# Performance work log

Measured on AMD Instinct MI355X. Metric: run time of the kernel, lower is better.

The kernel has to match this reference:

```python
import jax, jax.numpy as jnp
import numpy as np

N_GRAPHS = 512
N_PER_G = 84
N = N_GRAPHS * N_PER_G            # 43008 nodes
E = N_GRAPHS * N_PER_G * N_PER_G  # 3612672 edges (fully connected incl. self-loops)


def setup_inputs() -> dict:
    key = jax.random.key(0)
    ks = jax.random.split(key, 10)
    x = jax.random.normal(ks[0], (N, 84), dtype=jnp.float32)
    # fully-connected edge_index per graph: [2, E], row0=src j, row1=dst i
    off = (np.arange(N_GRAPHS) * N_PER_G)[:, None, None]
    src = (off + np.arange(N_PER_G)[:, None]) + np.zeros((1, 1, N_PER_G), np.int64)
    dst = (off + np.arange(N_PER_G)[None, None, :]) + np.zeros((1, N_PER_G, 1), np.int64)
    edge_index = jnp.asarray(np.stack([src.reshape(-1), dst.reshape(-1)]), dtype=jnp.int64)
    batch = jnp.asarray(np.repeat(np.arange(N_GRAPHS), N_PER_G), dtype=jnp.int64)
    s = 0.1
    W1 = jax.random.normal(ks[1], (84, 64), dtype=jnp.float32) * s
    a_src1 = jax.random.normal(ks[2], (32, 2), dtype=jnp.float32) * s
    a_dst1 = jax.random.normal(ks[3], (32, 2), dtype=jnp.float32) * s
    b1 = jnp.zeros((64,), jnp.float32)
    W2 = jax.random.normal(ks[4], (64, 64), dtype=jnp.float32) * s
    a_src2 = jax.random.normal(ks[5], (1, 64), dtype=jnp.float32) * s
    a_dst2 = jax.random.normal(ks[6], (1, 64), dtype=jnp.float32) * s
    b2 = jnp.zeros((64,), jnp.float32)
    Wfc = jax.random.normal(ks[7], (64, 1), dtype=jnp.float32) * s
    bfc = jnp.zeros((1,), jnp.float32)
    return {"x": x, "edge_index": edge_index, "batch": batch,
            "W1": W1, "a_src1": a_src1, "a_dst1": a_dst1, "b1": b1,
            "W2": W2, "a_src2": a_src2, "a_dst2": a_dst2, "b2": b2,
            "Wfc": Wfc, "bfc": bfc}


def gat_conv(x, W, a_src, a_dst, bias, src, dst, n_heads, ch):
    # x: [N, F] -> h: [N, H, C]
    h = (x @ W).reshape(-1, n_heads, ch)
    alpha_src = jnp.sum(h * a_src, axis=-1)  # [N, H]
    alpha_dst = jnp.sum(h * a_dst, axis=-1)  # [N, H]
    e = jax.nn.leaky_relu(alpha_src[src] + alpha_dst[dst], 0.2)  # [E, H]
    # segment softmax over edges grouped by destination node
    m = jax.ops.segment_max(e, dst, num_segments=N)
    e = jnp.exp(e - m[dst])
    z = jax.ops.segment_sum(e, dst, num_segments=N)
    alpha = e / (z[dst] + 1e-16)                              # [E, H]
    msg = h[src] * alpha[:, :, None]                          # [E, H, C]
    out = jax.ops.segment_sum(msg, dst, num_segments=N)       # [N, H, C]
    return out.reshape(-1, n_heads * ch) + bias


def reference(x, edge_index, batch, W1, a_src1, a_dst1, b1, W2, a_src2, a_dst2, b2, Wfc, bfc):
    src, dst = edge_index[0], edge_index[1]
    h = gat_conv(x, W1, a_src1, a_dst1, b1, src, dst, 32, 2)   # [N, 64]
    h = jax.nn.elu(h)
    h = gat_conv(h, W2, a_src2, a_dst2, b2, src, dst, 1, 64)   # [N, 64]
    # global mean pool per graph
    sums = jax.ops.segment_sum(h, batch, num_segments=N_GRAPHS)
    cnts = jax.ops.segment_sum(jnp.ones((N, 1), h.dtype), batch, num_segments=N_GRAPHS)
    pooled = sums / cnts                                       # [B, 64]
    out = pooled @ Wfc + bfc                                   # [B, 1]
    z = jnp.zeros((1,), jnp.float32)
    return (out, z, z, z, z, z, z)
```

## Files before the change

kernel.cpp:

```cpp
#include <hip/hip_runtime.h>

#define NG 512
#define P  84
#define F0 84
#define F1 64
#define L2E 1.4426950408889634f

typedef float f32x2 __attribute__((ext_vector_type(2)));

#if __has_builtin(__builtin_amdgcn_exp2f)
#define EXP2F(v) __builtin_amdgcn_exp2f(v)
#else
#define EXP2F(v) exp2f(v)
#endif
#if __has_builtin(__builtin_amdgcn_rcpf)
#define RCPF(v) __builtin_amdgcn_rcpf(v)
#else
#define RCPF(v) (1.0f / (v))
#endif

__device__ __forceinline__ float rlane(float v, int l) {
  return __int_as_float(__builtin_amdgcn_readlane(__float_as_int(v), l));
}


__launch_bounds__(512, 2)
__global__ void gat_fused(const float* __restrict__ x,
                          const float* __restrict__ W1,
                          const float* __restrict__ a_src1,
                          const float* __restrict__ a_dst1,
                          const float* __restrict__ b1,
                          const float* __restrict__ W2,
                          const float* __restrict__ a_src2,
                          const float* __restrict__ a_dst2,
                          const float* __restrict__ b2,
                          const float* __restrict__ Wfc,
                          const float* __restrict__ bfc,
                          float* __restrict__ out)
{
  __shared__ float  h1s[P * F1];
  __shared__ float  o1s[P * F1];
  __shared__ float  a2s[2 * F1];
  __shared__ float2 as2p[P];
  __shared__ float2 ad2p[P];
  __shared__ float  reds[8 * P];
  __shared__ float  redt[P];

  const int tid = threadIdx.x;
  const int ln  = tid & 63;
  const int wid = tid >> 6;
  const int g   = blockIdx.x;
  const int nrows = (wid < 4) ? 11 : 10;
  const int i0    = (wid < 4) ? wid * 11 : 44 + (wid - 4) * 10;

  if (g == 0 && tid < 6) out[NG + tid] = 0.f;

  const float* xg = x + (size_t)g * P * F0;

  float xr0[11], xr1[11];
  #pragma unroll
  for (int ii = 0; ii < 11; ++ii) {
    int ie = (ii < nrows) ? (i0 + ii) : i0;
    const float* xrow = xg + ie * F0;
    xr0[ii] = xrow[ln];
    xr1[ii] = (ln < F0 - 64) ? xrow[64 + ln] : 0.f;
  }
  if (tid < F1) a2s[tid] = a_src2[tid] * L2E;
  else if (tid < 2 * F1) a2s[tid] = a_dst2[tid - F1] * L2E;

  {
    float acc[11];
    #pragma unroll
    for (int ii = 0; ii < 11; ++ii) acc[ii] = 0.f;
    {
      float wk[42];
      #pragma unroll
      for (int k = 0; k < 42; ++k) wk[k] = W1[k * F1 + ln];
      #pragma unroll
      for (int k = 0; k < 42; ++k) {
        #pragma unroll
        for (int ii = 0; ii < 11; ++ii)
          acc[ii] = fmaf(rlane(xr0[ii], k), wk[k], acc[ii]);
      }
    }
    {
      float wk[42];
      #pragma unroll
      for (int k = 0; k < 42; ++k) wk[k] = W1[(42 + k) * F1 + ln];
      #pragma unroll
      for (int k = 0; k < 22; ++k) {
        #pragma unroll
        for (int ii = 0; ii < 11; ++ii)
          acc[ii] = fmaf(rlane(xr0[ii], 42 + k), wk[k], acc[ii]);
      }
      #pragma unroll
      for (int k = 0; k < 20; ++k) {
        #pragma unroll
        for (int ii = 0; ii < 11; ++ii)
          acc[ii] = fmaf(rlane(xr1[ii], k), wk[22 + k], acc[ii]);
      }
    }
    #pragma unroll
    for (int ii = 0; ii < 11; ++ii)
      if (ii < nrows) h1s[(i0 + ii) * F1 + ln] = acc[ii];
  }
  __syncthreads();

  {
    const int h  = tid & 31;
    const int ig = tid >> 5;
    const float asa = a_src1[2 * h] * L2E, asb = a_src1[2 * h + 1] * L2E;
    const float ada = a_dst1[2 * h] * L2E, adb = a_dst1[2 * h + 1] * L2E;
    f32x2 pi2[3], qi2[3], sm2[3], m02[3], m12[3];
    #pragma unroll
    for (int u = 0; u < 3; ++u) {
      int iA = ig + 16 * (2 * u);     if (iA >= P) iA = P - 1;
      int iB = ig + 16 * (2 * u + 1); if (iB >= P) iB = P - 1;
      float2 cA = *(const float2*)&h1s[iA * F1 + 2 * h];
      float2 cB = *(const float2*)&h1s[iB * F1 + 2 * h];
      float adiA = fmaf(cA.x, ada, cA.y * adb);
      float adiB = fmaf(cB.x, ada, cB.y * adb);
      pi2[u] = (f32x2){EXP2F(adiA), EXP2F(adiB)};
      qi2[u] = (f32x2){EXP2F(0.2f * adiA), EXP2F(0.2f * adiB)};
      sm2[u] = (f32x2){0.f, 0.f};
      m02[u] = (f32x2){0.f, 0.f};
      m12[u] = (f32x2){0.f, 0.f};
    }
    #pragma unroll 2
    for (int j = 0; j < P; ++j) {
      float2 c = *(const float2*)&h1s[j * F1 + 2 * h];
      float asj = fmaf(c.x, asa, c.y * asb);
      float ex = EXP2F(asj), ey = EXP2F(0.2f * asj);
      f32x2 exv = (f32x2){ex, ex}, eyv = (f32x2){ey, ey};
      f32x2 cxv = (f32x2){c.x, c.x}, cyv = (f32x2){c.y, c.y};
      #pragma unroll
      for (int u = 0; u < 3; ++u) {
        f32x2 p = __builtin_elementwise_max(exv * pi2[u], eyv * qi2[u]);
        sm2[u] += p;
        m02[u] += p * cxv;
        m12[u] += p * cyv;
      }
    }
    const float bc0 = b1[2 * h], bc1 = b1[2 * h + 1];
    #pragma unroll
    for (int u = 0; u < 3; ++u) {
      #pragma unroll
      for (int hf = 0; hf < 2; ++hf) {
        int i = ig + 16 * (2 * u + hf);
        if (i < P) {
          float rz = RCPF(sm2[u][hf]);
          float u0 = fmaf(m02[u][hf], rz, bc0);
          float u1 = fmaf(m12[u][hf], rz, bc1);
          u0 = u0 > 0.f ? u0 : (__expf(u0) - 1.f);
          u1 = u1 > 0.f ? u1 : (__expf(u1) - 1.f);
          float2 oo; oo.x = u0; oo.y = u1;
          *(float2*)&o1s[i * F1 + 2 * h] = oo;
        }
      }
    }
  }
  __syncthreads();

  {
    float or_[11];
    #pragma unroll
    for (int ii = 0; ii < 11; ++ii) {
      int ie = (ii < nrows) ? (i0 + ii) : i0;
      or_[ii] = o1s[ie * F1 + ln];
    }
    float acc[11];
    #pragma unroll
    for (int ii = 0; ii < 11; ++ii) acc[ii] = 0.f;
    {
      float wk[32];
      #pragma unroll
      for (int k = 0; k < 32; ++k) wk[k] = W2[k * F1 + ln];
      #pragma unroll
      for (int k = 0; k < 32; ++k) {
        #pragma unroll
        for (int ii = 0; ii < 11; ++ii)
          acc[ii] = fmaf(rlane(or_[ii], k), wk[k], acc[ii]);
      }
    }
    {
      float wk[32];
      #pragma unroll
      for (int k = 0; k < 32; ++k) wk[k] = W2[(32 + k) * F1 + ln];
      #pragma unroll
      for (int k = 0; k < 32; ++k) {
        #pragma unroll
        for (int ii = 0; ii < 11; ++ii)
          acc[ii] = fmaf(rlane(or_[ii], 32 + k), wk[k], acc[ii]);
      }
    }
    #pragma unroll
    for (int ii = 0; ii < 11; ++ii)
      if (ii < nrows) h1s[(i0 + ii) * F1 + ln] = acc[ii];
  }
  __syncthreads();

  if (tid < 2 * P) {
    const int n = tid >> 1, q = tid & 1;
    float s = 0.f, d = 0.f;
    #pragma unroll
    for (int t = 0; t < 32; ++t) {
      int f = q * 32 + ((t + n) & 31);
      float c = h1s[n * F1 + f];
      s = fmaf(c, a2s[f], s);
      d = fmaf(c, a2s[F1 + f], d);
    }
    s += __shfl_xor(s, 1, 64);
    d += __shfl_xor(d, 1, 64);
    if (q == 0) {
      float2 ps; ps.x = EXP2F(s); ps.y = EXP2F(0.2f * s);
      float2 pd; pd.x = EXP2F(d); pd.y = EXP2F(0.2f * d);
      as2p[n] = ps; ad2p[n] = pd;
    }
  }
  __syncthreads();

  {
    const float2 S0 = as2p[ln];
    float2 S1; S1.x = 0.f; S1.y = 0.f;
    if (ln < P - 64) S1 = as2p[64 + ln];
    float sj0 = 0.f, sj1 = 0.f;
    for (int ii = 0; ii < nrows; ++ii) {
      float2 D = ad2p[i0 + ii];
      float p0 = fmaxf(S0.x * D.x, S0.y * D.y);
      float p1 = (ln < P - 64) ? fmaxf(S1.x * D.x, S1.y * D.y) : 0.f;
      float ss = p0 + p1;
      #pragma unroll
      for (int off = 32; off > 0; off >>= 1) ss += __shfl_xor(ss, off, 64);
      float rz = RCPF(ss);
      sj0 = fmaf(p0, rz, sj0);
      sj1 = fmaf(p1, rz, sj1);
    }
    reds[wid * P + ln] = sj0;
    if (ln < P - 64) reds[wid * P + 64 + ln] = sj1;
  }
  __syncthreads();

  if (tid < P) {
    float s = 0.f;
    #pragma unroll
    for (int w = 0; w < 8; ++w) s += reds[w * P + tid];
    redt[tid] = s;
  }
  __syncthreads();

  if (wid == 0) {
    float c0 = 0.f, c1 = 0.f, c2 = 0.f, c3 = 0.f;
    for (int j = 0; j < P; j += 4) {
      c0 = fmaf(redt[j],     h1s[(j + 0) * F1 + ln], c0);
      c1 = fmaf(redt[j + 1], h1s[(j + 1) * F1 + ln], c1);
      c2 = fmaf(redt[j + 2], h1s[(j + 2) * F1 + ln], c2);
      c3 = fmaf(redt[j + 3], h1s[(j + 3) * F1 + ln], c3);
    }
    float pooled = ((c0 + c1) + (c2 + c3)) * (1.f / 84.f) + b2[ln];
    float v = pooled * Wfc[ln];
    #pragma unroll
    for (int off = 32; off > 0; off >>= 1) v += __shfl_xor(v, off, 64);
    if (ln == 0) out[g] = v + bfc[0];
  }
}

extern "C" void kernel_launch(void* const* d_in, const int* in_sizes, int n_in,
                              void* d_out, int out_size, void* d_ws, size_t ws_size,
                              hipStream_t stream) {
  const float* x      = (const float*)d_in[0];
  const float* W1     = (const float*)d_in[3];
  const float* a_src1 = (const float*)d_in[4];
  const float* a_dst1 = (const float*)d_in[5];
  const float* b1     = (const float*)d_in[6];
  const float* W2     = (const float*)d_in[7];
  const float* a_src2 = (const float*)d_in[8];
  const float* a_dst2 = (const float*)d_in[9];
  const float* b2     = (const float*)d_in[10];
  const float* Wfc    = (const float*)d_in[11];
  const float* bfc    = (const float*)d_in[12];
  hipLaunchKernelGGL(gat_fused, dim3(NG), dim3(512), 0, stream,
                     x, W1, a_src1, a_dst1, b1, W2, a_src2, a_dst2, b2, Wfc, bfc,
                     (float*)d_out);
}
```

Baseline: 156.3 us.

## Replace scalar readlane FMA projections with bf16 MFMA tiles staged in LDS

Both per-graph linear projections (x@W1 and o1@W2) were computed with per-lane FMAs fed by readlane broadcasts. They now use 16x16x32 bf16 MFMA instructions. Inputs, weights and the layer-1 output are converted to bf16 and staged in a padded shared buffer that also replaces the fp32 o1s buffer. This cuts VALU and readlane work and shared memory footprint, but adds conversion and staging cost and lowers the precision of both projections to bf16.

Result: faster. 128.3 us (-17.9%).

```diff
diff --git a/kernel.cpp b/kernel.cpp
--- a/kernel.cpp
+++ b/kernel.cpp
@@ -7,6 +7,8 @@
 #define L2E 1.4426950408889634f
 
 typedef float f32x2 __attribute__((ext_vector_type(2)));
+typedef float f32x4 __attribute__((ext_vector_type(4)));
+typedef short s16x8 __attribute__((ext_vector_type(8)));
 
 #if __has_builtin(__builtin_amdgcn_exp2f)
 #define EXP2F(v) __builtin_amdgcn_exp2f(v)
@@ -19,10 +21,18 @@
 #define RCPF(v) (1.0f / (v))
 #endif
 
-__device__ __forceinline__ float rlane(float v, int l) {
-  return __int_as_float(__builtin_amdgcn_readlane(__float_as_int(v), l));
+__device__ __forceinline__ unsigned short f2bf(float v) {
+  unsigned u = __float_as_uint(v);
+  u += 0x7FFF + ((u >> 16) & 1);
+  return (unsigned short)(u >> 16);
 }
 
+
+#define XPITCH   104
+#define W1T_OFF  (P * XPITCH)
+#define OPITCH   72
+#define W2T_OFF  (P * OPITCH)
+#define SBF_SZ   (P * XPITCH + F1 * XPITCH)
 
 __launch_bounds__(512, 2)
 __global__ void gat_fused(const float* __restrict__ x,
@@ -38,8 +48,8 @@
                           const float* __restrict__ bfc,
                           float* __restrict__ out)
 {
+  __shared__ __align__(16) unsigned short sbf[SBF_SZ];
   __shared__ float  h1s[P * F1];
-  __shared__ float  o1s[P * F1];
   __shared__ float  a2s[2 * F1];
   __shared__ float2 as2p[P];
   __shared__ float2 ad2p[P];
@@ -52,57 +62,66 @@
   const int g   = blockIdx.x;
   const int nrows = (wid < 4) ? 11 : 10;
   const int i0    = (wid < 4) ? wid * 11 : 44 + (wid - 4) * 10;
+  const int l15 = ln & 15, l4 = ln >> 4;
 
   if (g == 0 && tid < 6) out[NG + tid] = 0.f;
 
   const float* xg = x + (size_t)g * P * F0;
 
-  float xr0[11], xr1[11];
-  #pragma unroll
-  for (int ii = 0; ii < 11; ++ii) {
-    int ie = (ii < nrows) ? (i0 + ii) : i0;
-    const float* xrow = xg + ie * F0;
-    xr0[ii] = xrow[ln];
-    xr1[ii] = (ln < F0 - 64) ? xrow[64 + ln] : 0.f;
+  #pragma unroll
+  for (int t = 0; t < 14; ++t) {
+    int idx = tid + t * 512;
+    if (idx < P * F0) {
+      int i = (unsigned)idx / F0, k = idx - i * F0;
+      sbf[i * XPITCH + k] = f2bf(xg[idx]);
+    }
+  }
+  #pragma unroll
+  for (int t = 0; t < 2; ++t) {
+    int idx = tid + t * 512;
+    if (idx < P * 12) {
+      int i = (unsigned)idx / 12, k = idx - i * 12;
+      sbf[i * XPITCH + 84 + k] = 0;
+    }
+  }
+  #pragma unroll
+  for (int t = 0; t < 11; ++t) {
+    int idx = tid + t * 512;
+    if (idx < F0 * F1) {
+      int k = idx >> 6, f = idx & 63;
+      sbf[W1T_OFF + f * XPITCH + k] = f2bf(W1[idx]);
+    }
+  }
+  #pragma unroll
+  for (int t = 0; t < 2; ++t) {
+    int idx = tid + t * 512;
+    if (idx < F1 * 12) {
+      int f = (unsigned)idx / 12, k = idx - f * 12;
+      sbf[W1T_OFF + f * XPITCH + 84 + k] = 0;
+    }
   }
   if (tid < F1) a2s[tid] = a_src2[tid] * L2E;
   else if (tid < 2 * F1) a2s[tid] = a_dst2[tid - F1] * L2E;
-
-  {
-    float acc[11];
-    #pragma unroll
-    for (int ii = 0; ii < 11; ++ii) acc[ii] = 0.f;
-    {
-      float wk[42];
-      #pragma unroll
-      for (int k = 0; k < 42; ++k) wk[k] = W1[k * F1 + ln];
-      #pragma unroll
-      for (int k = 0; k < 42; ++k) {
-        #pragma unroll
-        for (int ii = 0; ii < 11; ++ii)
-          acc[ii] = fmaf(rlane(xr0[ii], k), wk[k], acc[ii]);
-      }
-    }
-    {
-      float wk[42];
-      #pragma unroll
-      for (int k = 0; k < 42; ++k) wk[k] = W1[(42 + k) * F1 + ln];
-      #pragma unroll
-      for (int k = 0; k < 22; ++k) {
-        #pragma unroll
-        for (int ii = 0; ii < 11; ++ii)
-          acc[ii] = fmaf(rlane(xr0[ii], 42 + k), wk[k], acc[ii]);
-      }
-      #pragma unroll
-      for (int k = 0; k < 20; ++k) {
-        #pragma unroll
-        for (int ii = 0; ii < 11; ++ii)
-          acc[ii] = fmaf(rlane(xr1[ii], k), wk[22 + k], acc[ii]);
-      }
-    }
-    #pragma unroll
-    for (int ii = 0; ii < 11; ++ii)
-      if (ii < nrows) h1s[(i0 + ii) * F1 + ln] = acc[ii];
+  __syncthreads();
+
+  #pragma unroll
+  for (int j = 0; j < 3; ++j) {
+    int t = wid * 3 + j;
+    int mt = t >> 2, nt = t & 3;
+    int row = mt * 16 + l15; if (row > P - 1) row = P - 1;
+    const int abase = row * XPITCH + l4 * 8;
+    const int bbase = W1T_OFF + (nt * 16 + l15) * XPITCH + l4 * 8;
+    f32x4 acc = {0.f, 0.f, 0.f, 0.f};
+    #pragma unroll
+    for (int ks = 0; ks < 3; ++ks) {
+      s16x8 af = *(const s16x8*)&sbf[abase + ks * 32];
+      s16x8 bf = *(const s16x8*)&sbf[bbase + ks * 32];
+      acc = __builtin_amdgcn_mfma_f32_16x16x32_bf16(af, bf, acc, 0, 0, 0);
+    }
+    int crow = mt * 16 + l4 * 4;
+    #pragma unroll
+    for (int v = 0; v < 4; ++v)
+      if (crow + v < P) h1s[(crow + v) * F1 + nt * 16 + l15] = acc[v];
   }
   __syncthreads();
 
@@ -153,49 +172,38 @@
           float u1 = fmaf(m12[u][hf], rz, bc1);
           u0 = u0 > 0.f ? u0 : (__expf(u0) - 1.f);
           u1 = u1 > 0.f ? u1 : (__expf(u1) - 1.f);
-          float2 oo; oo.x = u0; oo.y = u1;
-          *(float2*)&o1s[i * F1 + 2 * h] = oo;
+          unsigned pk = (unsigned)f2bf(u0) | ((unsigned)f2bf(u1) << 16);
+          *(unsigned*)&sbf[i * OPITCH + 2 * h] = pk;
         }
       }
     }
   }
-  __syncthreads();
-
-  {
-    float or_[11];
-    #pragma unroll
-    for (int ii = 0; ii < 11; ++ii) {
-      int ie = (ii < nrows) ? (i0 + ii) : i0;
-      or_[ii] = o1s[ie * F1 + ln];
-    }
-    float acc[11];
-    #pragma unroll
-    for (int ii = 0; ii < 11; ++ii) acc[ii] = 0.f;
-    {
-      float wk[32];
-      #pragma unroll
-      for (int k = 0; k < 32; ++k) wk[k] = W2[k * F1 + ln];
-      #pragma unroll
-      for (int k = 0; k < 32; ++k) {
-        #pragma unroll
-        for (int ii = 0; ii < 11; ++ii)
-          acc[ii] = fmaf(rlane(or_[ii], k), wk[k], acc[ii]);
-      }
-    }
-    {
-      float wk[32];
-      #pragma unroll
-      for (int k = 0; k < 32; ++k) wk[k] = W2[(32 + k) * F1 + ln];
-      #pragma unroll
-      for (int k = 0; k < 32; ++k) {
-        #pragma unroll
-        for (int ii = 0; ii < 11; ++ii)
-          acc[ii] = fmaf(rlane(or_[ii], 32 + k), wk[k], acc[ii]);
-      }
-    }
-    #pragma unroll
-    for (int ii = 0; ii < 11; ++ii)
-      if (ii < nrows) h1s[(i0 + ii) * F1 + ln] = acc[ii];
+  #pragma unroll
+  for (int t = 0; t < 8; ++t) {
+    int idx = tid + t * 512;
+    int k = idx >> 6, f = idx & 63;
+    sbf[W2T_OFF + f * OPITCH + k] = f2bf(W2[idx]);
+  }
+  __syncthreads();
+
+  #pragma unroll
+  for (int j = 0; j < 3; ++j) {
+    int t = wid * 3 + j;
+    int mt = t >> 2, nt = t & 3;
+    int row = mt * 16 + l15; if (row > P - 1) row = P - 1;
+    const int abase = row * OPITCH + l4 * 8;
+    const int bbase = W2T_OFF + (nt * 16 + l15) * OPITCH + l4 * 8;
+    f32x4 acc = {0.f, 0.f, 0.f, 0.f};
+    #pragma unroll
+    for (int ks = 0; ks < 2; ++ks) {
+      s16x8 af = *(const s16x8*)&sbf[abase + ks * 32];
+      s16x8 bf = *(const s16x8*)&sbf[bbase + ks * 32];
+      acc = __builtin_amdgcn_mfma_f32_16x16x32_bf16(af, bf, acc, 0, 0, 0);
+    }
+    int crow = mt * 16 + l4 * 4;
+    #pragma unroll
+    for (int v = 0; v < 4; ++v)
+      if (crow + v < P) h1s[(crow + v) * F1 + nt * 16 + l15] = acc[v];
   }
   __syncthreads();
 
```
